# Kernel optimization log

Hardware: AMD Instinct MI355X
Metric: run time of the kernel (lower is better)

Reference implementation:

```python
import jax, jax.numpy as jnp
import numpy as np

N_PATCH = 4194304  # H*W with H=W=2048
H_GT, W_GT = 2050, 2050  # gt padded by 1 on each side


def setup_inputs() -> dict:
    key = jax.random.key(0)
    k1, k2, k3 = jax.random.split(key, 3)
    image = jax.random.uniform(k1, (N_PATCH, 3, 3), dtype=jnp.float32)
    edges_prob = jax.random.uniform(k2, (N_PATCH, 3, 3), dtype=jnp.float32)
    gt = jax.random.uniform(k3, (H_GT, W_GT), dtype=jnp.float32)
    return {"image": image, "edges_prob": edges_prob, "gt": gt}


def reference(image, edges_prob, gt):
    # image: [N,3,3], edges_prob: [N,3,3], gt: [H+2, W+2]
    N = image.shape[0]
    img = image.reshape(N, 9)
    edg = edges_prob.reshape(N, 9)

    # Per-patch segment reduce: edg==0 -> ignored; edg>0.5 -> disacc; else -> acc
    m_dis = edg > 0.5
    m_acc = (edg != 0.0) & ~m_dis
    c_dis = m_dis.sum(axis=-1)
    c_acc = m_acc.sum(axis=-1)
    md = (img * m_dis).sum(axis=-1) / jnp.maximum(c_dis, 1)  # mean of disacc group
    ma = (img * m_acc).sum(axis=-1) / jnp.maximum(c_acc, 1)  # mean of acc group
    valid = (c_dis > 0) & (c_acc > 0)

    # 0 = black, 1 = white, 2 = unknown
    out = jnp.where(valid, jnp.where(md > ma, 0.0, 1.0), 2.0)

    # Global masked means of center pixels over black / white classes
    values = image[:, 1, 1]
    mb = (out == 0.0)
    mw = (out == 1.0)
    avgB = (values * mb).sum() / jnp.maximum(mb.sum(), 1)
    avgW = (values * mw).sum() / jnp.maximum(mw.sum(), 1)

    # Correction: resolve unknowns by nearest class average
    corr = jnp.where(
        out == 2.0,
        jnp.where(jnp.abs(values - avgB) < jnp.abs(values - avgW), 0.0, 1.0),
        out,
    )

    H = gt.shape[0] - 2
    W = gt.shape[1] - 2
    return corr.reshape(H, W)
```

## Files before the change

kernel.cpp:

```cpp
#include <hip/hip_runtime.h>


struct Partial { float sb, sw; unsigned int cb, cw; };
struct Acc     { double sumB, sumW; unsigned int cntB, cntW; };

#define PPB    256
#define CHUNKS 4
#define NBLK1  4096

__global__ __launch_bounds__(256) void phase1(const float* __restrict__ img,
                                              const float* __restrict__ edg,
                                              float* __restrict__ out,
                                              Partial* __restrict__ part)
{
    __shared__ float s_img[PPB * 9];
    __shared__ float s_edg[PPB * 9];
    const int t = threadIdx.x;

    float accB = 0.0f, accW = 0.0f;
    int   ncb = 0, ncw = 0;

    for (int c = 0; c < CHUNKS; ++c) {
        const size_t chunk = (size_t)blockIdx.x * CHUNKS + c;
        const size_t base  = chunk * (PPB * 9);

        const float4* gi = reinterpret_cast<const float4*>(img + base);
        const float4* ge = reinterpret_cast<const float4*>(edg + base);
        float4* si = reinterpret_cast<float4*>(s_img);
        float4* se = reinterpret_cast<float4*>(s_edg);
        si[t]       = gi[t];       se[t]       = ge[t];
        si[t + 256] = gi[t + 256]; se[t + 256] = ge[t + 256];
        if (t < 64) { si[t + 512] = gi[t + 512]; se[t + 512] = ge[t + 512]; }
        __syncthreads();

        const float* ip = s_img + 9 * t;
        const float* ep = s_edg + 9 * t;

        float xd[9], xa[9];
        int cd = 0, ca = 0;
#pragma unroll
        for (int k = 0; k < 9; ++k) {
            float e = ep[k], v = ip[k];
            bool dis = e > 0.5f;
            bool ac  = (e != 0.0f) && !dis;
            xd[k] = dis ? v : 0.0f;
            xa[k] = ac  ? v : 0.0f;
            cd += dis ? 1 : 0;
            ca += ac  ? 1 : 0;
        }
        float sd = ((xd[0] + xd[1]) + (xd[2] + xd[3])) + ((xd[4] + xd[5]) + (xd[6] + xd[7]));
        sd += xd[8];
        float sa = ((xa[0] + xa[1]) + (xa[2] + xa[3])) + ((xa[4] + xa[5]) + (xa[6] + xa[7]));
        sa += xa[8];

        const int cdm = cd > 0 ? cd : 1;
        const int cam = ca > 0 ? ca : 1;
        const bool gt = ((double)sd * (double)cam) > ((double)sa * (double)cdm);
        const float o = (cd > 0 && ca > 0) ? (gt ? 0.0f : 1.0f) : 2.0f;
        const float value = ip[4];

        out[chunk * PPB + t] = o;

        accB += (o == 0.0f) ? value : 0.0f;
        accW += (o == 1.0f) ? value : 0.0f;
        ncb  += (o == 0.0f) ? 1 : 0;
        ncw  += (o == 1.0f) ? 1 : 0;

        __syncthreads();
    }

#pragma unroll
    for (int off = 32; off > 0; off >>= 1) {
        accB += __shfl_down(accB, off);
        accW += __shfl_down(accW, off);
        ncb  += __shfl_down(ncb, off);
        ncw  += __shfl_down(ncw, off);
    }
    __shared__ float rb[4], rw[4];
    __shared__ unsigned int ub[4], uw[4];
    const int wave = t >> 6, lane = t & 63;
    if (lane == 0) { rb[wave] = accB; rw[wave] = accW; ub[wave] = ncb; uw[wave] = ncw; }
    __syncthreads();
    if (t == 0) {
        Partial p;
        p.sb = (rb[0] + rb[1]) + (rb[2] + rb[3]);
        p.sw = (rw[0] + rw[1]) + (rw[2] + rw[3]);
        p.cb = ub[0] + ub[1] + ub[2] + ub[3];
        p.cw = uw[0] + uw[1] + uw[2] + uw[3];
        part[blockIdx.x] = p;
    }
}

__global__ __launch_bounds__(256) void reduceK(const Partial* __restrict__ part,
                                               int n, Acc* __restrict__ acc)
{
    const int t = threadIdx.x;
    double sb = 0.0, sw = 0.0;
    unsigned int cb = 0, cw = 0;
    for (int i = t; i < n; i += 256) {
        Partial p = part[i];
        sb += (double)p.sb; sw += (double)p.sw; cb += p.cb; cw += p.cw;
    }
#pragma unroll
    for (int off = 32; off > 0; off >>= 1) {
        sb += __shfl_down(sb, off);
        sw += __shfl_down(sw, off);
        cb += __shfl_down(cb, off);
        cw += __shfl_down(cw, off);
    }
    __shared__ double db[4], dw[4];
    __shared__ unsigned int eb[4], ew[4];
    const int wave = t >> 6, lane = t & 63;
    if (lane == 0) { db[wave] = sb; dw[wave] = sw; eb[wave] = cb; ew[wave] = cw; }
    __syncthreads();
    if (t == 0) {
        Acc a;
        a.sumB = db[0] + db[1] + db[2] + db[3];
        a.sumW = dw[0] + dw[1] + dw[2] + dw[3];
        a.cntB = eb[0] + eb[1] + eb[2] + eb[3];
        a.cntW = ew[0] + ew[1] + ew[2] + ew[3];
        *acc = a;
    }
}

__global__ __launch_bounds__(256) void phase2(const float* __restrict__ img,
                                              float* __restrict__ out,
                                              const Acc* __restrict__ acc,
                                              int n4)
{
    const int i = blockIdx.x * 256 + threadIdx.x;
    if (i >= n4) return;
    float4 v = reinterpret_cast<const float4*>(out)[i];
    if (v.x == 2.0f || v.y == 2.0f || v.z == 2.0f || v.w == 2.0f) {
        const unsigned cb = acc->cntB, cw = acc->cntW;
        const double avgB = acc->sumB / (double)(cb ? cb : 1u);
        const double avgW = acc->sumW / (double)(cw ? cw : 1u);
        float r[4] = {v.x, v.y, v.z, v.w};
#pragma unroll
        for (int j = 0; j < 4; ++j) {
            if (r[j] == 2.0f) {
                const size_t p = (size_t)i * 4 + j;
                const double val = (double)img[p * 9 + 4];
                out[p] = (fabs(val - avgB) < fabs(val - avgW)) ? 0.0f : 1.0f;
            }
        }
    }
}

extern "C" void kernel_launch(void* const* d_in, const int* in_sizes, int n_in,
                              void* d_out, int out_size, void* d_ws, size_t ws_size,
                              hipStream_t stream) {
    const float* img = (const float*)d_in[0];
    const float* edg = (const float*)d_in[1];
    float* out = (float*)d_out;

    Partial* part = (Partial*)d_ws;
    Acc*     acc  = (Acc*)((char*)d_ws + NBLK1 * sizeof(Partial));

    const int N = in_sizes[0] / 9;
    phase1<<<NBLK1, 256, 0, stream>>>(img, edg, out, part);
    reduceK<<<1, 256, 0, stream>>>(part, NBLK1, acc);
    const int n4 = N / 4;
    phase2<<<(n4 + 255) / 256, 256, 0, stream>>>(img, out, acc, n4);
}
```

Measured before the change: 69.88 us.

## Load four patches per thread directly into registers, dropping LDS staging

```diff
diff --git a/kernel.cpp b/kernel.cpp
--- a/kernel.cpp
+++ b/kernel.cpp
@@ -4,37 +4,38 @@
 struct Partial { float sb, sw; unsigned int cb, cw; };
 struct Acc     { double sumB, sumW; unsigned int cntB, cntW; };
 
-#define PPB    256
-#define CHUNKS 4
-#define NBLK1  4096
+#define NBLK1 4096
 
 __global__ __launch_bounds__(256) void phase1(const float* __restrict__ img,
                                               const float* __restrict__ edg,
                                               float* __restrict__ out,
                                               Partial* __restrict__ part)
 {
-    __shared__ float s_img[PPB * 9];
-    __shared__ float s_edg[PPB * 9];
     const int t = threadIdx.x;
+    const size_t tid = (size_t)blockIdx.x * 256 + t;
+
+    const float4* gi = reinterpret_cast<const float4*>(img) + tid * 9;
+    const float4* ge = reinterpret_cast<const float4*>(edg) + tid * 9;
+    float im[36], ed[36];
+#pragma unroll
+    for (int j = 0; j < 9; ++j) {
+        float4 a = gi[j];
+        im[4*j] = a.x; im[4*j+1] = a.y; im[4*j+2] = a.z; im[4*j+3] = a.w;
+    }
+#pragma unroll
+    for (int j = 0; j < 9; ++j) {
+        float4 b = ge[j];
+        ed[4*j] = b.x; ed[4*j+1] = b.y; ed[4*j+2] = b.z; ed[4*j+3] = b.w;
+    }
 
     float accB = 0.0f, accW = 0.0f;
     int   ncb = 0, ncw = 0;
+    float o4[4];
 
-    for (int c = 0; c < CHUNKS; ++c) {
-        const size_t chunk = (size_t)blockIdx.x * CHUNKS + c;
-        const size_t base  = chunk * (PPB * 9);
-
-        const float4* gi = reinterpret_cast<const float4*>(img + base);
-        const float4* ge = reinterpret_cast<const float4*>(edg + base);
-        float4* si = reinterpret_cast<float4*>(s_img);
-        float4* se = reinterpret_cast<float4*>(s_edg);
-        si[t]       = gi[t];       se[t]       = ge[t];
-        si[t + 256] = gi[t + 256]; se[t + 256] = ge[t + 256];
-        if (t < 64) { si[t + 512] = gi[t + 512]; se[t + 512] = ge[t + 512]; }
-        __syncthreads();
-
-        const float* ip = s_img + 9 * t;
-        const float* ep = s_edg + 9 * t;
+#pragma unroll
+    for (int p = 0; p < 4; ++p) {
+        const float* ip = im + 9 * p;
+        const float* ep = ed + 9 * p;
 
         float xd[9], xa[9];
         int cd = 0, ca = 0;
@@ -59,15 +60,15 @@
         const float o = (cd > 0 && ca > 0) ? (gt ? 0.0f : 1.0f) : 2.0f;
         const float value = ip[4];
 
-        out[chunk * PPB + t] = o;
-
+        o4[p] = o;
         accB += (o == 0.0f) ? value : 0.0f;
         accW += (o == 1.0f) ? value : 0.0f;
         ncb  += (o == 0.0f) ? 1 : 0;
         ncw  += (o == 1.0f) ? 1 : 0;
+    }
 
-        __syncthreads();
-    }
+    float4 ov = make_float4(o4[0], o4[1], o4[2], o4[3]);
+    reinterpret_cast<float4*>(out)[tid] = ov;
 
 #pragma unroll
     for (int off = 32; off > 0; off >>= 1) {
```

Result: slower. 78.56 us (+12.4%).

## Fuse classify, reduce and correction into one cooperative kernel with grid sync

Applied to the files above, without the earlier changes.

```diff
diff --git a/kernel.cpp b/kernel.cpp
--- a/kernel.cpp
+++ b/kernel.cpp
@@ -1,28 +1,58 @@
 #include <hip/hip_runtime.h>
+#include <hip/hip_cooperative_groups.h>
+
+namespace cg = cooperative_groups;
 
 
 struct Partial { float sb, sw; unsigned int cb, cw; };
 struct Acc     { double sumB, sumW; unsigned int cntB, cntW; };
 
-#define PPB    256
-#define CHUNKS 4
-#define NBLK1  4096
-
-__global__ __launch_bounds__(256) void phase1(const float* __restrict__ img,
-                                              const float* __restrict__ edg,
-                                              float* __restrict__ out,
-                                              Partial* __restrict__ part)
-{
-    __shared__ float s_img[PPB * 9];
-    __shared__ float s_edg[PPB * 9];
+#define NBLKC  1024
+#define CHUNKS 16
+
+__device__ __forceinline__ int classify(const float* ip, const float* ep, float& value) {
+    float xd[9], xa[9];
+    int cd = 0, ca = 0;
+#pragma unroll
+    for (int k = 0; k < 9; ++k) {
+        float e = ep[k], v = ip[k];
+        bool dis = e > 0.5f;
+        bool ac  = (e != 0.0f) && !dis;
+        xd[k] = dis ? v : 0.0f;
+        xa[k] = ac  ? v : 0.0f;
+        cd += dis ? 1 : 0;
+        ca += ac  ? 1 : 0;
+    }
+    float sd = ((xd[0] + xd[1]) + (xd[2] + xd[3])) + ((xd[4] + xd[5]) + (xd[6] + xd[7]));
+    sd += xd[8];
+    float sa = ((xa[0] + xa[1]) + (xa[2] + xa[3])) + ((xa[4] + xa[5]) + (xa[6] + xa[7]));
+    sa += xa[8];
+    const int cdm = cd > 0 ? cd : 1;
+    const int cam = ca > 0 ? ca : 1;
+    const bool gt = ((double)sd * (double)cam) > ((double)sa * (double)cdm);
+    value = ip[4];
+    return (cd > 0 && ca > 0) ? (gt ? 0 : 1) : 2;
+}
+
+__global__ __launch_bounds__(256, 4) void fused(const float* __restrict__ img,
+                                                const float* __restrict__ edg,
+                                                float* __restrict__ out,
+                                                Partial* __restrict__ part,
+                                                Acc* __restrict__ acc)
+{
+    __shared__ float s_img[256 * 9];
+    __shared__ float s_edg[256 * 9];
     const int t = threadIdx.x;
 
+    float val[CHUNKS];
+    unsigned int ocode = 0;
     float accB = 0.0f, accW = 0.0f;
     int   ncb = 0, ncw = 0;
 
+#pragma unroll
     for (int c = 0; c < CHUNKS; ++c) {
         const size_t chunk = (size_t)blockIdx.x * CHUNKS + c;
-        const size_t base  = chunk * (PPB * 9);
+        const size_t base  = chunk * (256 * 9);
 
         const float4* gi = reinterpret_cast<const float4*>(img + base);
         const float4* ge = reinterpret_cast<const float4*>(edg + base);
@@ -33,39 +63,126 @@
         if (t < 64) { si[t + 512] = gi[t + 512]; se[t + 512] = ge[t + 512]; }
         __syncthreads();
 
-        const float* ip = s_img + 9 * t;
-        const float* ep = s_edg + 9 * t;
-
-        float xd[9], xa[9];
-        int cd = 0, ca = 0;
-#pragma unroll
-        for (int k = 0; k < 9; ++k) {
-            float e = ep[k], v = ip[k];
-            bool dis = e > 0.5f;
-            bool ac  = (e != 0.0f) && !dis;
-            xd[k] = dis ? v : 0.0f;
-            xa[k] = ac  ? v : 0.0f;
-            cd += dis ? 1 : 0;
-            ca += ac  ? 1 : 0;
-        }
-        float sd = ((xd[0] + xd[1]) + (xd[2] + xd[3])) + ((xd[4] + xd[5]) + (xd[6] + xd[7]));
-        sd += xd[8];
-        float sa = ((xa[0] + xa[1]) + (xa[2] + xa[3])) + ((xa[4] + xa[5]) + (xa[6] + xa[7]));
-        sa += xa[8];
-
-        const int cdm = cd > 0 ? cd : 1;
-        const int cam = ca > 0 ? ca : 1;
-        const bool gt = ((double)sd * (double)cam) > ((double)sa * (double)cdm);
-        const float o = (cd > 0 && ca > 0) ? (gt ? 0.0f : 1.0f) : 2.0f;
-        const float value = ip[4];
-
-        out[chunk * PPB + t] = o;
-
-        accB += (o == 0.0f) ? value : 0.0f;
-        accW += (o == 1.0f) ? value : 0.0f;
-        ncb  += (o == 0.0f) ? 1 : 0;
-        ncw  += (o == 1.0f) ? 1 : 0;
-
+        float v;
+        int code = classify(s_img + 9 * t, s_edg + 9 * t, v);
+        val[c] = v;
+        ocode |= (unsigned)code << (2 * c);
+
+        accB += (code == 0) ? v : 0.0f;
+        accW += (code == 1) ? v : 0.0f;
+        ncb  += (code == 0) ? 1 : 0;
+        ncw  += (code == 1) ? 1 : 0;
+
+        __syncthreads();
+    }
+
+#pragma unroll
+    for (int off = 32; off > 0; off >>= 1) {
+        accB += __shfl_down(accB, off);
+        accW += __shfl_down(accW, off);
+        ncb  += __shfl_down(ncb, off);
+        ncw  += __shfl_down(ncw, off);
+    }
+    {
+        __shared__ float rb[4], rw[4];
+        __shared__ unsigned int ub[4], uw[4];
+        const int wave = t >> 6, lane = t & 63;
+        if (lane == 0) { rb[wave] = accB; rw[wave] = accW; ub[wave] = ncb; uw[wave] = ncw; }
+        __syncthreads();
+        if (t == 0) {
+            Partial p;
+            p.sb = (rb[0] + rb[1]) + (rb[2] + rb[3]);
+            p.sw = (rw[0] + rw[1]) + (rw[2] + rw[3]);
+            p.cb = ub[0] + ub[1] + ub[2] + ub[3];
+            p.cw = uw[0] + uw[1] + uw[2] + uw[3];
+            part[blockIdx.x] = p;
+        }
+    }
+
+    cg::this_grid().sync();
+
+    if (blockIdx.x == 0) {
+        double sb = 0.0, sw = 0.0;
+        unsigned int cb = 0, cw = 0;
+#pragma unroll
+        for (int i = 0; i < NBLKC; i += 256) {
+            Partial p = part[i + t];
+            sb += (double)p.sb; sw += (double)p.sw; cb += p.cb; cw += p.cw;
+        }
+#pragma unroll
+        for (int off = 32; off > 0; off >>= 1) {
+            sb += __shfl_down(sb, off);
+            sw += __shfl_down(sw, off);
+            cb += __shfl_down(cb, off);
+            cw += __shfl_down(cw, off);
+        }
+        __shared__ double db[4], dw[4];
+        __shared__ unsigned int eb[4], ew[4];
+        const int wave = t >> 6, lane = t & 63;
+        if (lane == 0) { db[wave] = sb; dw[wave] = sw; eb[wave] = cb; ew[wave] = cw; }
+        __syncthreads();
+        if (t == 0) {
+            Acc a;
+            a.sumB = db[0] + db[1] + db[2] + db[3];
+            a.sumW = dw[0] + dw[1] + dw[2] + dw[3];
+            a.cntB = eb[0] + eb[1] + eb[2] + eb[3];
+            a.cntW = ew[0] + ew[1] + ew[2] + ew[3];
+            *acc = a;
+        }
+    }
+
+    cg::this_grid().sync();
+
+    const unsigned cb = acc->cntB, cw = acc->cntW;
+    const double avgB = acc->sumB / (double)(cb ? cb : 1u);
+    const double avgW = acc->sumW / (double)(cw ? cw : 1u);
+
+#pragma unroll
+    for (int c = 0; c < CHUNKS; ++c) {
+        const size_t chunk = (size_t)blockIdx.x * CHUNKS + c;
+        const int code = (ocode >> (2 * c)) & 3;
+        float o;
+        if (code == 2) {
+            const double v = (double)val[c];
+            o = (fabs(v - avgB) < fabs(v - avgW)) ? 0.0f : 1.0f;
+        } else {
+            o = (float)code;
+        }
+        out[chunk * 256 + t] = o;
+    }
+}
+
+
+__global__ __launch_bounds__(256) void phase1(const float* __restrict__ img,
+                                              const float* __restrict__ edg,
+                                              float* __restrict__ out,
+                                              Partial* __restrict__ part)
+{
+    __shared__ float s_img[256 * 9];
+    __shared__ float s_edg[256 * 9];
+    const int t = threadIdx.x;
+    float accB = 0.0f, accW = 0.0f;
+    int   ncb = 0, ncw = 0;
+
+    for (int c = 0; c < 4; ++c) {
+        const size_t chunk = (size_t)blockIdx.x * 4 + c;
+        const size_t base  = chunk * (256 * 9);
+        const float4* gi = reinterpret_cast<const float4*>(img + base);
+        const float4* ge = reinterpret_cast<const float4*>(edg + base);
+        float4* si = reinterpret_cast<float4*>(s_img);
+        float4* se = reinterpret_cast<float4*>(s_edg);
+        si[t]       = gi[t];       se[t]       = ge[t];
+        si[t + 256] = gi[t + 256]; se[t + 256] = ge[t + 256];
+        if (t < 64) { si[t + 512] = gi[t + 512]; se[t + 512] = ge[t + 512]; }
+        __syncthreads();
+
+        float v;
+        int code = classify(s_img + 9 * t, s_edg + 9 * t, v);
+        out[chunk * 256 + t] = (float)code;
+        accB += (code == 0) ? v : 0.0f;
+        accW += (code == 1) ? v : 0.0f;
+        ncb  += (code == 0) ? 1 : 0;
+        ncw  += (code == 1) ? 1 : 0;
         __syncthreads();
     }
 
@@ -155,11 +272,17 @@
     float* out = (float*)d_out;
 
     Partial* part = (Partial*)d_ws;
-    Acc*     acc  = (Acc*)((char*)d_ws + NBLK1 * sizeof(Partial));
+    Acc*     acc  = (Acc*)((char*)d_ws + 4096 * sizeof(Partial));
 
     const int N = in_sizes[0] / 9;
-    phase1<<<NBLK1, 256, 0, stream>>>(img, edg, out, part);
-    reduceK<<<1, 256, 0, stream>>>(part, NBLK1, acc);
-    const int n4 = N / 4;
-    phase2<<<(n4 + 255) / 256, 256, 0, stream>>>(img, out, acc, n4);
-}
+
+    void* args[] = { (void*)&img, (void*)&edg, (void*)&out, (void*)&part, (void*)&acc };
+    hipError_t e = hipLaunchCooperativeKernel((const void*)fused, dim3(NBLKC), dim3(256),
+                                              args, 0, stream);
+    if (e != hipSuccess) {
+        phase1<<<4096, 256, 0, stream>>>(img, edg, out, part);
+        reduceK<<<1, 256, 0, stream>>>(part, 4096, acc);
+        const int n4 = N / 4;
+        phase2<<<(n4 + 255) / 256, 256, 0, stream>>>(img, out, acc, n4);
+    }
+}
```

Result: slower. 277.8 us (+297.6%).
